# Performance work log

Hardware: AMD Instinct MI355X
Metric: run time of the kernel (lower is better)

## Reference

```python
import jax, jax.numpy as jnp
import numpy as np

D_MODEL = 1024
NUM_HEADS = 16
HEAD_DIM = D_MODEL // NUM_HEADS


def setup_inputs() -> dict:
    key = jax.random.key(0)
    kq, kk, kv, kw, kb = jax.random.split(key, 5)
    N, S = 2, 2048
    query = jax.random.normal(kq, (N, S, D_MODEL), dtype=jnp.float32)
    key_t = jax.random.normal(kk, (N, S, D_MODEL), dtype=jnp.float32)
    value = jax.random.normal(kv, (N, S, D_MODEL), dtype=jnp.float32)
    # fc_out params (nn.Linear(d_model, d_model)): W [out,in], b [out]
    lim = 1.0 / np.sqrt(D_MODEL)
    W_out = jax.random.uniform(kw, (D_MODEL, D_MODEL), minval=-lim, maxval=lim, dtype=jnp.float32)
    b_out = jax.random.uniform(kb, (D_MODEL,), minval=-lim, maxval=lim, dtype=jnp.float32)
    return {"query": query, "key": key_t, "value": value, "W_out": W_out, "b_out": b_out}


def reference(query, key, value, W_out, b_out):
    N, Lq, _ = query.shape
    Lk = key.shape[1]
    q = query.reshape(N, Lq, NUM_HEADS, HEAD_DIM)
    k = key.reshape(N, Lk, NUM_HEADS, HEAD_DIM)
    v = value.reshape(N, Lk, NUM_HEADS, HEAD_DIM)
    # NOTE: original module does NOT apply q/k/v Linear layers and does NOT scale by 1/sqrt(d)
    scores = jnp.einsum("nqhd,nkhd->nhqk", q, k)
    attn = jax.nn.softmax(scores, axis=3)
    out = jnp.einsum("nhqk,nkhd->nqhd", attn, v).reshape(N, Lq, D_MODEL)
    return out @ W_out.T + b_out
```

## Files before the change

### kernel.cpp

```cpp
#include <hip/hip_runtime.h>

typedef _Float16 half8 __attribute__((ext_vector_type(8)));
typedef _Float16 half4 __attribute__((ext_vector_type(4)));
typedef float f32x4 __attribute__((ext_vector_type(4)));
typedef float f32x16 __attribute__((ext_vector_type(16)));
typedef unsigned u32x4 __attribute__((ext_vector_type(4)));

#define N_B 2
#define S_LEN 2048
#define NH 16
#define HD 64
#define DM 1024
#define LOG2E 1.44269504088896f

__device__ __forceinline__ void gload16(const void* g, void* l) {
    __builtin_amdgcn_global_load_lds(
        (const __attribute__((address_space(1))) unsigned int*)g,
        (__attribute__((address_space(3))) unsigned int*)l, 16, 0, 0);
}

__device__ __forceinline__ float fexp2(float x) {
    float r;
    asm("v_exp_f32 %0, %1" : "=v"(r) : "v"(x));
    return r;
}

__global__ __launch_bounds__(256) void k_prep(const float* __restrict__ K,
                                              const float* __restrict__ V,
                                              const float* __restrict__ Wo,
                                              _Float16* __restrict__ Kh,
                                              _Float16* __restrict__ Vt,
                                              _Float16* __restrict__ Wh) {
    __shared__ _Float16 tile[64][65];
    const int id = blockIdx.x;
    if (id < 4096) {
        int i = id * 256 + threadIdx.x;
        float4 v = ((const float4*)K)[i];
        int base = i * 4;
        int d = base & 63;
        int h = (base >> 6) & 15;
        int s = (base >> 10) & 2047;
        int n = base >> 21;
        size_t o = ((size_t)((n * NH + h) * S_LEN + s)) * HD + d;
        half4 hv = {(_Float16)v.x, (_Float16)v.y, (_Float16)v.z, (_Float16)v.w};
        *(half4*)(Kh + o) = hv;
    } else if (id < 5120) {
        int b = id - 4096;
        int st = b & 31, h = (b >> 5) & 15, n = b >> 9;
        int c = threadIdx.x & 63, r0 = threadIdx.x >> 6;
#pragma unroll
        for (int i = 0; i < 16; ++i) {
            int r = i * 4 + r0;
            tile[r][c] = (_Float16)V[((size_t)(n * S_LEN) + st * 64 + r) * DM + h * HD + c];
        }
        __syncthreads();
#pragma unroll
        for (int i = 0; i < 16; ++i) {
            int d = i * 4 + r0;
            Vt[((size_t)((n * NH + h) * HD + d)) * S_LEN + st * 64 + c] = tile[c][d];
        }
    } else {
        int i = (id - 5120) * 256 + threadIdx.x;
        float4 v = ((const float4*)Wo)[i];
        half4 hv = {(_Float16)v.x, (_Float16)v.y, (_Float16)v.z, (_Float16)v.w};
        *(half4*)(Wh + (size_t)i * 4) = hv;
    }
}

__global__ __launch_bounds__(512, 4) void k_attn(const float* __restrict__ Q,
                                                 const _Float16* __restrict__ Kh,
                                                 const _Float16* __restrict__ Vth,
                                                 _Float16* __restrict__ Oatt) {
    __shared__ char SB[65536];

    const int id = blockIdx.x;
    const int xcd = id & 7;
    const int sl = id >> 3;
    const int nh = xcd + 8 * (sl >> 4);
    const int qt = sl & 15;

    const int tid = threadIdx.x;
    const int w = tid >> 6;
    const int wq = w & 3;
    const int hf = w >> 2;
    const int lane = tid & 63;
    const int l31 = lane & 31;
    const int hi = lane >> 5;
    const int n = nh >> 4, h = nh & 15;

    const size_t head = (size_t)nh * S_LEN * HD;
    const char* Khead = (const char*)(Kh + head);
    const char* Vhead = (const char*)(Vth + head);

    const int qg = qt * 128 + wq * 32 + l31;
    const float* qbase = Q + ((size_t)(n * S_LEN) + qg) * DM + h * HD;
    auto mkqf = [&](int c) -> half8 {
        float4 a = *(const float4*)(qbase + 16 * c + 8 * hi);
        float4 b = *(const float4*)(qbase + 16 * c + 8 * hi + 4);
        half8 r = {(_Float16)(a.x * LOG2E), (_Float16)(a.y * LOG2E),
                   (_Float16)(a.z * LOG2E), (_Float16)(a.w * LOG2E),
                   (_Float16)(b.x * LOG2E), (_Float16)(b.y * LOG2E),
                   (_Float16)(b.z * LOG2E), (_Float16)(b.w * LOG2E)};
        return r;
    };
    half8 qf0 = mkqf(0), qf1 = mkqf(1), qf2 = mkqf(2), qf3 = mkqf(3);

    f32x16 oacc0 = {}, oacc1 = {};
    float m_q = -1e30f, l_q = 0.f;

    const int rr = lane >> 3;
    const int cb = (lane & 7) * 16;
    const int gcb = cb ^ (rr << 4);

    auto kbuf = [&](int b, int half) -> char* { return SB + (b * 2 + half) * 8192; };
    auto vbuf = [&](int b, int half) -> char* { return SB + 32768 + (b * 2 + half) * 8192; };

    auto STAGE = [&](int t, int b) {
#pragma unroll
        for (int j = 0; j < 2; ++j) {
            int slice = wq * 2 + j;
            int row = slice * 8 + rr;
            int key = hf * 1024 + t * 64 + row;
            gload16(Khead + (size_t)key * 128 + gcb, kbuf(b, hf) + slice * 1024);
            gload16(Vhead + (size_t)row * 4096 + hf * 2048 + t * 128 + gcb,
                    vbuf(b, hf) + slice * 1024);
        }
    };

    const int rmask = (l31 & 7) << 4;
    auto ldF = [&](const char* lds, int blk, int c) -> half8 {
        int off = (32 * blk + l31) * 128 + ((32 * c + 16 * hi) ^ rmask);
        return *(const half8*)(lds + off);
    };

    auto pk2 = [&](float a, float b) -> unsigned {
        unsigned short ua = __builtin_bit_cast(unsigned short, (_Float16)a);
        unsigned short ub = __builtin_bit_cast(unsigned short, (_Float16)b);
        return (unsigned)ua | ((unsigned)ub << 16);
    };
    auto mkpa = [&](const f32x16& S, int rb) -> half8 {
        unsigned w0 = pk2(S[rb + 0], S[rb + 1]);
        unsigned w1 = pk2(S[rb + 2], S[rb + 3]);
        unsigned w2 = pk2(S[rb + 4], S[rb + 5]);
        unsigned w3 = pk2(S[rb + 6], S[rb + 7]);
        unsigned x0 = (unsigned)__shfl_xor((int)w0, 32);
        unsigned x1 = (unsigned)__shfl_xor((int)w1, 32);
        unsigned x2 = (unsigned)__shfl_xor((int)w2, 32);
        unsigned x3 = (unsigned)__shfl_xor((int)w3, 32);
        u32x4 t;
        t[0] = hi ? x2 : w0;
        t[1] = hi ? x3 : w1;
        t[2] = hi ? w2 : x0;
        t[3] = hi ? w3 : x1;
        return __builtin_bit_cast(half8, t);
    };

    auto BODY = [&](int t, int buf, bool do_stage) {
        if (do_stage) STAGE(t + 1, buf ^ 1);
        const char* ldsK = kbuf(buf, hf);
        const char* ldsV = vbuf(buf, hf);

        f32x16 s0 = {}, s1 = {};
        s0 = __builtin_amdgcn_mfma_f32_32x32x16_f16(ldF(ldsK, 0, 0), qf0, s0, 0, 0, 0);
        s0 = __builtin_amdgcn_mfma_f32_32x32x16_f16(ldF(ldsK, 0, 1), qf1, s0, 0, 0, 0);
        s0 = __builtin_amdgcn_mfma_f32_32x32x16_f16(ldF(ldsK, 0, 2), qf2, s0, 0, 0, 0);
        s0 = __builtin_amdgcn_mfma_f32_32x32x16_f16(ldF(ldsK, 0, 3), qf3, s0, 0, 0, 0);
        s1 = __builtin_amdgcn_mfma_f32_32x32x16_f16(ldF(ldsK, 1, 0), qf0, s1, 0, 0, 0);
        s1 = __builtin_amdgcn_mfma_f32_32x32x16_f16(ldF(ldsK, 1, 1), qf1, s1, 0, 0, 0);
        s1 = __builtin_amdgcn_mfma_f32_32x32x16_f16(ldF(ldsK, 1, 2), qf2, s1, 0, 0, 0);
        s1 = __builtin_amdgcn_mfma_f32_32x32x16_f16(ldF(ldsK, 1, 3), qf3, s1, 0, 0, 0);

        float mx[16];
#pragma unroll
        for (int i = 0; i < 16; ++i) mx[i] = fmaxf(s0[i], s1[i]);
#pragma unroll
        for (int st = 8; st > 0; st >>= 1)
#pragma unroll
            for (int i = 0; i < 8; ++i)
                if (i < st) mx[i] = fmaxf(mx[i], mx[i + st]);
        float tm = fmaxf(mx[0], __shfl_xor(mx[0], 32));
        if (!__all(tm <= m_q + 8.f)) {
            float mn = fmaxf(m_q, tm);
            float sc = fexp2(m_q - mn);
            m_q = mn;
            l_q *= sc;
            int scb = __builtin_bit_cast(int, sc);
#pragma unroll
            for (int r = 0; r < 16; ++r) {
                int qr = (r & 3) + 8 * (r >> 2) + 4 * hi;
                float s = __builtin_bit_cast(float, __builtin_amdgcn_ds_bpermute(4 * qr, scb));
                oacc0[r] *= s;
                oacc1[r] *= s;
            }
        }
        float rs = 0.f;
#pragma unroll
        for (int i = 0; i < 16; ++i) { float p = fexp2(s0[i] - m_q); s0[i] = p; rs += p; }
#pragma unroll
        for (int i = 0; i < 16; ++i) { float p = fexp2(s1[i] - m_q); s1[i] = p; rs += p; }
        rs += __shfl_xor(rs, 32);
        l_q += rs;

        half8 pa0 = mkpa(s0, 0), pa1 = mkpa(s0, 8);
        half8 pa2 = mkpa(s1, 0), pa3 = mkpa(s1, 8);

        oacc0 = __builtin_amdgcn_mfma_f32_32x32x16_f16(pa0, ldF(ldsV, 0, 0), oacc0, 0, 0, 0);
        oacc0 = __builtin_amdgcn_mfma_f32_32x32x16_f16(pa1, ldF(ldsV, 0, 1), oacc0, 0, 0, 0);
        oacc0 = __builtin_amdgcn_mfma_f32_32x32x16_f16(pa2, ldF(ldsV, 0, 2), oacc0, 0, 0, 0);
        oacc0 = __builtin_amdgcn_mfma_f32_32x32x16_f16(pa3, ldF(ldsV, 0, 3), oacc0, 0, 0, 0);
        oacc1 = __builtin_amdgcn_mfma_f32_32x32x16_f16(pa0, ldF(ldsV, 1, 0), oacc1, 0, 0, 0);
        oacc1 = __builtin_amdgcn_mfma_f32_32x32x16_f16(pa1, ldF(ldsV, 1, 1), oacc1, 0, 0, 0);
        oacc1 = __builtin_amdgcn_mfma_f32_32x32x16_f16(pa2, ldF(ldsV, 1, 2), oacc1, 0, 0, 0);
        oacc1 = __builtin_amdgcn_mfma_f32_32x32x16_f16(pa3, ldF(ldsV, 1, 3), oacc1, 0, 0, 0);

        if (do_stage) __syncthreads();
    };

    STAGE(0, 0);
    __syncthreads();
    for (int t = 0; t < 15; ++t) BODY(t, t & 1, true);
    BODY(15, 1, false);

    __syncthreads();
    float* MRG = (float*)SB;
    if (hf == 1) {
        float* B = MRG + wq * 2176;
        B[lane] = m_q;
        B[64 + lane] = l_q;
#pragma unroll
        for (int r = 0; r < 16; ++r) {
            B[128 + r * 64 + lane] = oacc0[r];
            B[1152 + r * 64 + lane] = oacc1[r];
        }
    }
    __syncthreads();
    if (hf == 0) {
        float* B = MRG + wq * 2176;
        float m1 = B[lane], l1 = B[64 + lane];
        float m = fmaxf(m_q, m1);
        float e0 = fexp2(m_q - m), e1 = fexp2(m1 - m);
        float linv = 1.f / (l_q * e0 + l1 * e1);
        int e0b = __builtin_bit_cast(int, e0);
        int e1b = __builtin_bit_cast(int, e1);
        int ivb = __builtin_bit_cast(int, linv);
#pragma unroll
        for (int r = 0; r < 16; ++r) {
            int qr = (r & 3) + 8 * (r >> 2) + 4 * hi;
            float s0f = __builtin_bit_cast(float, __builtin_amdgcn_ds_bpermute(4 * qr, e0b));
            float s1f = __builtin_bit_cast(float, __builtin_amdgcn_ds_bpermute(4 * qr, e1b));
            float iv = __builtin_bit_cast(float, __builtin_amdgcn_ds_bpermute(4 * qr, ivb));
            float o0 = (oacc0[r] * s0f + B[128 + r * 64 + lane] * s1f) * iv;
            float o1 = (oacc1[r] * s0f + B[1152 + r * 64 + lane] * s1f) * iv;
            int qglob = qt * 128 + wq * 32 + qr;
            size_t base = ((size_t)(n * S_LEN + qglob)) * DM + h * HD + l31;
            Oatt[base] = (_Float16)o0;
            Oatt[base + 32] = (_Float16)o1;
        }
    }
}

__global__ __launch_bounds__(256) void k_proj(const _Float16* __restrict__ A,
                                              const _Float16* __restrict__ W,
                                              const float* __restrict__ bias,
                                              float* __restrict__ out) {
    __shared__ _Float16 As[2][128 * 64];
    __shared__ _Float16 Ws[2][128 * 64];

    const int id = blockIdx.x;
    const int ot = id & 7;
    const int mt = id >> 3;
    const int tid = threadIdx.x;
    const int w = tid >> 6;
    const int lane = tid & 63;
    const int lr = lane & 15, lg = lane >> 4;
    const int wm = (w >> 1) * 64, wn = (w & 1) * 64;

    const int rr = lane >> 3;
    const int cb = (lane & 7) * 16;
    const int gcb = cb ^ (rr << 4);

    const char* Abase = (const char*)(A + (size_t)(mt * 128) * DM);
    const char* Wbase = (const char*)(W + (size_t)(ot * 128) * DM);

    auto STAGE = [&](int kt, int b) {
#pragma unroll
        for (int r = 0; r < 4; ++r) {
            int row = r * 32 + w * 8 + rr;
            gload16(Abase + (size_t)row * 2048 + kt * 128 + gcb,
                    (char*)&As[b][0] + (r * 32 + w * 8) * 128);
            gload16(Wbase + (size_t)row * 2048 + kt * 128 + gcb,
                    (char*)&Ws[b][0] + (r * 32 + w * 8) * 128);
        }
    };

    f32x4 zero = {0.f, 0.f, 0.f, 0.f};
    f32x4 acc[4][4];
#pragma unroll
    for (int mi = 0; mi < 4; ++mi)
#pragma unroll
        for (int ni = 0; ni < 4; ++ni) acc[mi][ni] = zero;

    auto COMPUTE = [&](int b) {
        const char* ldsA = (const char*)&As[b][0];
        const char* ldsW = (const char*)&Ws[b][0];
        half8 af[4][2], wf[4][2];
#pragma unroll
        for (int mi = 0; mi < 4; ++mi) {
            int row = wm + mi * 16 + lr;
            int sw = (row & 7) << 4;
            const char* p = ldsA + row * 128;
            af[mi][0] = *(const half8*)(p + ((lg * 16) ^ sw));
            af[mi][1] = *(const half8*)(p + ((64 + lg * 16) ^ sw));
        }
#pragma unroll
        for (int ni = 0; ni < 4; ++ni) {
            int row = wn + ni * 16 + lr;
            int sw = (row & 7) << 4;
            const char* p = ldsW + row * 128;
            wf[ni][0] = *(const half8*)(p + ((lg * 16) ^ sw));
            wf[ni][1] = *(const half8*)(p + ((64 + lg * 16) ^ sw));
        }
#pragma unroll
        for (int mi = 0; mi < 4; ++mi)
#pragma unroll
            for (int ni = 0; ni < 4; ++ni) {
                acc[mi][ni] = __builtin_amdgcn_mfma_f32_16x16x32_f16(af[mi][0], wf[ni][0], acc[mi][ni], 0, 0, 0);
                acc[mi][ni] = __builtin_amdgcn_mfma_f32_16x16x32_f16(af[mi][1], wf[ni][1], acc[mi][ni], 0, 0, 0);
            }
    };

    STAGE(0, 0);
    __syncthreads();
    for (int kt = 0; kt < 15; ++kt) {
        STAGE(kt + 1, (kt & 1) ^ 1);
        COMPUTE(kt & 1);
        __syncthreads();
    }
    COMPUTE(1);

#pragma unroll
    for (int ni = 0; ni < 4; ++ni) {
        int o = ot * 128 + wn + ni * 16 + lr;
        float b = bias[o];
#pragma unroll
        for (int mi = 0; mi < 4; ++mi)
#pragma unroll
            for (int i = 0; i < 4; ++i) {
                int m = mt * 128 + wm + mi * 16 + lg * 4 + i;
                out[(size_t)m * DM + o] = acc[mi][ni][i] + b;
            }
    }
}

extern "C" void kernel_launch(void* const* d_in, const int* in_sizes, int n_in,
                              void* d_out, int out_size, void* d_ws, size_t ws_size,
                              hipStream_t stream) {
    const float* Q = (const float*)d_in[0];
    const float* K = (const float*)d_in[1];
    const float* V = (const float*)d_in[2];
    const float* Wo = (const float*)d_in[3];
    const float* bo = (const float*)d_in[4];
    float* out = (float*)d_out;
    char* ws = (char*)d_ws;

    _Float16* Kh = (_Float16*)(ws);
    _Float16* Vt = (_Float16*)(ws + (8u << 20));
    _Float16* Oatt = (_Float16*)(ws + (16u << 20));
    _Float16* Wh = (_Float16*)(ws + (24u << 20));

    k_prep<<<6144, 256, 0, stream>>>(K, V, Wo, Kh, Vt, Wh);
    k_attn<<<512, 512, 0, stream>>>(Q, Kh, Vt, Oatt);
    k_proj<<<256, 256, 0, stream>>>(Oatt, Wh, bo, out);
}
```

Baseline: 98.35 us.

## Single-buffer V tile with mid-iteration barrier and MFMA priority hints

Measured after the change: 99.22 us. Within noise of the previous version (+0.9%).

```diff
diff --git a/kernel.cpp b/kernel.cpp
--- a/kernel.cpp
+++ b/kernel.cpp
@@ -71,7 +71,7 @@
                                                  const _Float16* __restrict__ Kh,
                                                  const _Float16* __restrict__ Vth,
                                                  _Float16* __restrict__ Oatt) {
-    __shared__ char SB[65536];
+    __shared__ char SB[49152];
 
     const int id = blockIdx.x;
     const int xcd = id & 7;
@@ -113,17 +113,24 @@
     const int gcb = cb ^ (rr << 4);
 
     auto kbuf = [&](int b, int half) -> char* { return SB + (b * 2 + half) * 8192; };
-    auto vbuf = [&](int b, int half) -> char* { return SB + 32768 + (b * 2 + half) * 8192; };
-
-    auto STAGE = [&](int t, int b) {
+    auto vbuf = [&](int half) -> char* { return SB + 32768 + half * 8192; };
+
+    auto STAGE_K = [&](int t, int b) {
 #pragma unroll
         for (int j = 0; j < 2; ++j) {
             int slice = wq * 2 + j;
             int row = slice * 8 + rr;
             int key = hf * 1024 + t * 64 + row;
             gload16(Khead + (size_t)key * 128 + gcb, kbuf(b, hf) + slice * 1024);
+        }
+    };
+    auto STAGE_V = [&](int t) {
+#pragma unroll
+        for (int j = 0; j < 2; ++j) {
+            int slice = wq * 2 + j;
+            int row = slice * 8 + rr;
             gload16(Vhead + (size_t)row * 4096 + hf * 2048 + t * 128 + gcb,
-                    vbuf(b, hf) + slice * 1024);
+                    vbuf(hf) + slice * 1024);
         }
     };
 
@@ -155,12 +162,17 @@
         return __builtin_bit_cast(half8, t);
     };
 
-    auto BODY = [&](int t, int buf, bool do_stage) {
-        if (do_stage) STAGE(t + 1, buf ^ 1);
+    STAGE_K(0, 0);
+    __syncthreads();
+
+    for (int t = 0; t < 16; ++t) {
+        const int buf = t & 1;
+        STAGE_V(t);
+        if (t < 15) STAGE_K(t + 1, buf ^ 1);
         const char* ldsK = kbuf(buf, hf);
-        const char* ldsV = vbuf(buf, hf);
 
         f32x16 s0 = {}, s1 = {};
+        __builtin_amdgcn_s_setprio(1);
         s0 = __builtin_amdgcn_mfma_f32_32x32x16_f16(ldF(ldsK, 0, 0), qf0, s0, 0, 0, 0);
         s0 = __builtin_amdgcn_mfma_f32_32x32x16_f16(ldF(ldsK, 0, 1), qf1, s0, 0, 0, 0);
         s0 = __builtin_amdgcn_mfma_f32_32x32x16_f16(ldF(ldsK, 0, 2), qf2, s0, 0, 0, 0);
@@ -169,6 +181,7 @@
         s1 = __builtin_amdgcn_mfma_f32_32x32x16_f16(ldF(ldsK, 1, 1), qf1, s1, 0, 0, 0);
         s1 = __builtin_amdgcn_mfma_f32_32x32x16_f16(ldF(ldsK, 1, 2), qf2, s1, 0, 0, 0);
         s1 = __builtin_amdgcn_mfma_f32_32x32x16_f16(ldF(ldsK, 1, 3), qf3, s1, 0, 0, 0);
+        __builtin_amdgcn_s_setprio(0);
 
         float mx[16];
 #pragma unroll
@@ -204,6 +217,10 @@
         half8 pa0 = mkpa(s0, 0), pa1 = mkpa(s0, 8);
         half8 pa2 = mkpa(s1, 0), pa3 = mkpa(s1, 8);
 
+        __syncthreads();
+
+        const char* ldsV = vbuf(hf);
+        __builtin_amdgcn_s_setprio(1);
         oacc0 = __builtin_amdgcn_mfma_f32_32x32x16_f16(pa0, ldF(ldsV, 0, 0), oacc0, 0, 0, 0);
         oacc0 = __builtin_amdgcn_mfma_f32_32x32x16_f16(pa1, ldF(ldsV, 0, 1), oacc0, 0, 0, 0);
         oacc0 = __builtin_amdgcn_mfma_f32_32x32x16_f16(pa2, ldF(ldsV, 0, 2), oacc0, 0, 0, 0);
@@ -212,16 +229,11 @@
         oacc1 = __builtin_amdgcn_mfma_f32_32x32x16_f16(pa1, ldF(ldsV, 1, 1), oacc1, 0, 0, 0);
         oacc1 = __builtin_amdgcn_mfma_f32_32x32x16_f16(pa2, ldF(ldsV, 1, 2), oacc1, 0, 0, 0);
         oacc1 = __builtin_amdgcn_mfma_f32_32x32x16_f16(pa3, ldF(ldsV, 1, 3), oacc1, 0, 0, 0);
-
-        if (do_stage) __syncthreads();
-    };
-
-    STAGE(0, 0);
-    __syncthreads();
-    for (int t = 0; t < 15; ++t) BODY(t, t & 1, true);
-    BODY(15, 1, false);
-
-    __syncthreads();
+        __builtin_amdgcn_s_setprio(0);
+
+        __syncthreads();
+    }
+
     float* MRG = (float*)SB;
     if (hf == 1) {
         float* B = MRG + wq * 2176;
```
